# Kernel tuning notes

Hardware: AMD Instinct MI355X
Metric: run time of the kernel (lower is better)

Reference implementation:

```python
import jax, jax.numpy as jnp
import numpy as np

# SMPL-X kinematic tree (55 joints): parent index per joint, root = -1
PARENTS = np.array([-1, 0, 0, 0, 1, 2, 3, 4, 5, 6, 7, 8, 9, 9, 9, 12, 13, 14,
                    16, 17, 18, 19, 15, 22, 23, 20, 25, 26, 20, 28, 29, 20, 31,
                    32, 20, 34, 35, 20, 37, 38, 21, 40, 41, 21, 43, 44, 21, 46,
                    47, 21, 49, 50, 21, 52, 53], dtype=np.int32)
N_JOINTS = 55
B, T = 32, 2048


def setup_inputs() -> dict:
    key = jax.random.key(0)
    k1, k2 = jax.random.split(key)
    motion = jax.random.normal(k1, (B, T, N_JOINTS, 3, 3), dtype=jnp.float32)
    J = jax.random.normal(k2, (N_JOINTS, 3), dtype=jnp.float32) * 0.2  # rest-pose joints
    return {"motion": motion, "J": J}


def reference(motion, J):
    """Process_3D_Motion.calculate_pos with ignore_joints=[].

    motion: [B, T, N, 3, 3] per-joint rotation matrices
    J:      [N, 3] rest-pose joint locations
    returns posed joint positions [B, T, N, 3] (batch_rigid_transform).
    """
    b, t, n = motion.shape[:3]
    bt = b * t
    rot = motion.reshape(bt, n, 3, 3)

    # relative joint offsets w.r.t. parent (root stays absolute)
    rel = jnp.concatenate([J[:1], J[1:] - J[PARENTS[1:]]], axis=0)  # [N, 3]

    # build homogeneous 4x4 transforms [BT, N, 4, 4]
    trans = jnp.broadcast_to(rel[None, :, :, None], (bt, n, 3, 1))
    top = jnp.concatenate([rot, trans], axis=-1)                    # [BT, N, 3, 4]
    bottom_row = jnp.array([0.0, 0.0, 0.0, 1.0], dtype=motion.dtype)
    bottom = jnp.broadcast_to(bottom_row[None, None, None, :], (bt, n, 1, 4))
    mats = jnp.concatenate([top, bottom], axis=-2)                  # [BT, N, 4, 4]

    # sequential kinematic-chain composition (fixed, small loop over joints)
    chain = [mats[:, 0]]
    for i in range(1, n):
        chain.append(chain[int(PARENTS[i])] @ mats[:, i])
    transforms = jnp.stack(chain, axis=1)                           # [BT, N, 4, 4]

    posed = transforms[:, :, :3, 3]                                 # [BT, N, 3]
    return posed.reshape(b, t, n, 3)
```

## Files before the change

kernel.cpp:

```cpp
#include <hip/hip_runtime.h>

#define NJ 55

__device__ constexpr int kPar[NJ] = {
    -1, 0, 0, 0, 1, 2, 3, 4, 5, 6, 7, 8, 9, 9, 9, 12, 13, 14, 16, 17,
    18, 19, 15, 22, 23, 20, 25, 26, 20, 28, 29, 20, 31, 32, 20, 34, 35,
    20, 37, 38, 21, 40, 41, 21, 43, 44, 21, 46, 47, 21, 49, 50, 21, 52, 53
};

__global__ __launch_bounds__(256)
void fk_kernel(const float* __restrict__ motion,
               const float* __restrict__ Jrest,
               float* __restrict__ out,
               int BT)
{
    __shared__ float rel[NJ * 3];

    if (threadIdx.x < NJ) {
        const int j = threadIdx.x;
        const int p = kPar[j];
        float x = Jrest[j * 3 + 0];
        float y = Jrest[j * 3 + 1];
        float z = Jrest[j * 3 + 2];
        if (p >= 0) {
            x -= Jrest[p * 3 + 0];
            y -= Jrest[p * 3 + 1];
            z -= Jrest[p * 3 + 2];
        }
        rel[j * 3 + 0] = x;
        rel[j * 3 + 1] = y;
        rel[j * 3 + 2] = z;
    }
    __syncthreads();

    const int g = blockIdx.x * blockDim.x + threadIdx.x;
    if (g >= BT) return;

    const float* __restrict__ m = motion + (size_t)g * (NJ * 9);
    float* __restrict__ o = out + (size_t)g * (NJ * 3);

    float R[NJ][9];
    float t[NJ][3];

#pragma unroll
    for (int j = 0; j < NJ; ++j) {
        const float b0 = m[j * 9 + 0];
        const float b1 = m[j * 9 + 1];
        const float b2 = m[j * 9 + 2];
        const float b3 = m[j * 9 + 3];
        const float b4 = m[j * 9 + 4];
        const float b5 = m[j * 9 + 5];
        const float b6 = m[j * 9 + 6];
        const float b7 = m[j * 9 + 7];
        const float b8 = m[j * 9 + 8];

        const float rx = rel[j * 3 + 0];
        const float ry = rel[j * 3 + 1];
        const float rz = rel[j * 3 + 2];

        const int p = kPar[j];
        if (p < 0) {
            R[j][0] = b0; R[j][1] = b1; R[j][2] = b2;
            R[j][3] = b3; R[j][4] = b4; R[j][5] = b5;
            R[j][6] = b6; R[j][7] = b7; R[j][8] = b8;
            t[j][0] = rx;
            t[j][1] = ry;
            t[j][2] = rz;
        } else {
            const float a0 = R[p][0], a1 = R[p][1], a2 = R[p][2];
            const float a3 = R[p][3], a4 = R[p][4], a5 = R[p][5];
            const float a6 = R[p][6], a7 = R[p][7], a8 = R[p][8];

            R[j][0] = a0 * b0 + a1 * b3 + a2 * b6;
            R[j][1] = a0 * b1 + a1 * b4 + a2 * b7;
            R[j][2] = a0 * b2 + a1 * b5 + a2 * b8;
            R[j][3] = a3 * b0 + a4 * b3 + a5 * b6;
            R[j][4] = a3 * b1 + a4 * b4 + a5 * b7;
            R[j][5] = a3 * b2 + a4 * b5 + a5 * b8;
            R[j][6] = a6 * b0 + a7 * b3 + a8 * b6;
            R[j][7] = a6 * b1 + a7 * b4 + a8 * b7;
            R[j][8] = a6 * b2 + a7 * b5 + a8 * b8;

            t[j][0] = a0 * rx + a1 * ry + a2 * rz + t[p][0];
            t[j][1] = a3 * rx + a4 * ry + a5 * rz + t[p][1];
            t[j][2] = a6 * rx + a7 * ry + a8 * rz + t[p][2];
        }

        o[j * 3 + 0] = t[j][0];
        o[j * 3 + 1] = t[j][1];
        o[j * 3 + 2] = t[j][2];
    }
}

extern "C" void kernel_launch(void* const* d_in, const int* in_sizes, int n_in,
                              void* d_out, int out_size, void* d_ws, size_t ws_size,
                              hipStream_t stream) {
    const float* motion = (const float*)d_in[0];
    const float* Jrest  = (const float*)d_in[1];
    float* out = (float*)d_out;

    const int BT = in_sizes[0] / (NJ * 9);

    const int block = 256;
    const int grid = (BT + block - 1) / block;
    fk_kernel<<<grid, block, 0, stream>>>(motion, Jrest, out, BT);
}
```

Before: 262.8 us.

## Stage motion tiles into LDS with async double-buffered loads and coalesced stores

```diff
diff --git a/kernel.cpp b/kernel.cpp
--- a/kernel.cpp
+++ b/kernel.cpp
@@ -1,6 +1,12 @@
 #include <hip/hip_runtime.h>
+#include <stdint.h>
 
-#define NJ 55
+#define NJ   55
+#define JT   5
+#define NT   11
+#define SPB  64
+#define TFL  (JT * 9)
+#define OFL  (JT * 3)
 
 __device__ constexpr int kPar[NJ] = {
     -1, 0, 0, 0, 1, 2, 3, 4, 5, 6, 7, 8, 9, 9, 9, 12, 13, 14, 16, 17,
@@ -8,88 +14,128 @@
     20, 37, 38, 21, 40, 41, 21, 43, 44, 21, 46, 47, 21, 49, 50, 21, 52, 53
 };
 
-__global__ __launch_bounds__(256)
+typedef const __attribute__((address_space(1))) void glb_v;
+typedef __attribute__((address_space(3))) void lds_v;
+
+__global__ __launch_bounds__(64)
 void fk_kernel(const float* __restrict__ motion,
                const float* __restrict__ Jrest,
                float* __restrict__ out,
                int BT)
 {
-    __shared__ float rel[NJ * 3];
+    __shared__ float lds_in[2][SPB * TFL];
+    __shared__ float lds_out[SPB * OFL];
+    __shared__ float lds_rel[NJ * 3];
 
-    if (threadIdx.x < NJ) {
-        const int j = threadIdx.x;
-        const int p = kPar[j];
-        float x = Jrest[j * 3 + 0];
-        float y = Jrest[j * 3 + 1];
-        float z = Jrest[j * 3 + 2];
+    const int lane  = threadIdx.x;
+    const int blk_s = blockIdx.x * SPB;
+
+    if (lane < NJ) {
+        const int p = kPar[lane];
+        float x = Jrest[lane * 3 + 0];
+        float y = Jrest[lane * 3 + 1];
+        float z = Jrest[lane * 3 + 2];
         if (p >= 0) {
             x -= Jrest[p * 3 + 0];
             y -= Jrest[p * 3 + 1];
             z -= Jrest[p * 3 + 2];
         }
-        rel[j * 3 + 0] = x;
-        rel[j * 3 + 1] = y;
-        rel[j * 3 + 2] = z;
+        lds_rel[lane * 3 + 0] = x;
+        lds_rel[lane * 3 + 1] = y;
+        lds_rel[lane * 3 + 2] = z;
     }
     __syncthreads();
 
-    const int g = blockIdx.x * blockDim.x + threadIdx.x;
-    if (g >= BT) return;
+    const float* __restrict__ mbase = motion + (size_t)blk_s * (NJ * 9);
 
-    const float* __restrict__ m = motion + (size_t)g * (NJ * 9);
-    float* __restrict__ o = out + (size_t)g * (NJ * 3);
+#define STAGE(T, BUF)                                                        \
+    do {                                                                     \
+        _Pragma("unroll")                                                    \
+        for (int it = 0; it < TFL; ++it) {                                   \
+            const int idx = it * SPB + lane;                                 \
+            const int s   = idx / TFL;              \
+            const int e   = idx - s * TFL;                                   \
+            const float* gp = mbase + (size_t)s * (NJ * 9) + (T) * TFL + e;  \
+            __builtin_amdgcn_global_load_lds(                                \
+                (glb_v*)gp, (lds_v*)&lds_in[BUF][it * SPB], 4, 0, 0);        \
+        }                                                                    \
+    } while (0)
 
-    float R[NJ][9];
-    float t[NJ][3];
+    float Rw[NJ][9];
+    float tw[NJ][3];
+
+    STAGE(0, 0);
 
 #pragma unroll
-    for (int j = 0; j < NJ; ++j) {
-        const float b0 = m[j * 9 + 0];
-        const float b1 = m[j * 9 + 1];
-        const float b2 = m[j * 9 + 2];
-        const float b3 = m[j * 9 + 3];
-        const float b4 = m[j * 9 + 4];
-        const float b5 = m[j * 9 + 5];
-        const float b6 = m[j * 9 + 6];
-        const float b7 = m[j * 9 + 7];
-        const float b8 = m[j * 9 + 8];
+    for (int t = 0; t < NT; ++t) {
+        if (t < NT - 1) {
+            STAGE(t + 1, (t + 1) & 1);
+            asm volatile("s_waitcnt vmcnt(45)" ::: "memory");
+        } else {
+            asm volatile("s_waitcnt vmcnt(0)" ::: "memory");
+        }
+        __builtin_amdgcn_sched_barrier(0);
 
-        const float rx = rel[j * 3 + 0];
-        const float ry = rel[j * 3 + 1];
-        const float rz = rel[j * 3 + 2];
+        const float* __restrict__ Lin = &lds_in[t & 1][0];
 
-        const int p = kPar[j];
-        if (p < 0) {
-            R[j][0] = b0; R[j][1] = b1; R[j][2] = b2;
-            R[j][3] = b3; R[j][4] = b4; R[j][5] = b5;
-            R[j][6] = b6; R[j][7] = b7; R[j][8] = b8;
-            t[j][0] = rx;
-            t[j][1] = ry;
-            t[j][2] = rz;
-        } else {
-            const float a0 = R[p][0], a1 = R[p][1], a2 = R[p][2];
-            const float a3 = R[p][3], a4 = R[p][4], a5 = R[p][5];
-            const float a6 = R[p][6], a7 = R[p][7], a8 = R[p][8];
+#pragma unroll
+        for (int q = 0; q < JT; ++q) {
+            const int j = t * JT + q;
 
-            R[j][0] = a0 * b0 + a1 * b3 + a2 * b6;
-            R[j][1] = a0 * b1 + a1 * b4 + a2 * b7;
-            R[j][2] = a0 * b2 + a1 * b5 + a2 * b8;
-            R[j][3] = a3 * b0 + a4 * b3 + a5 * b6;
-            R[j][4] = a3 * b1 + a4 * b4 + a5 * b7;
-            R[j][5] = a3 * b2 + a4 * b5 + a5 * b8;
-            R[j][6] = a6 * b0 + a7 * b3 + a8 * b6;
-            R[j][7] = a6 * b1 + a7 * b4 + a8 * b7;
-            R[j][8] = a6 * b2 + a7 * b5 + a8 * b8;
+            const float b0 = Lin[lane * TFL + q * 9 + 0];
+            const float b1 = Lin[lane * TFL + q * 9 + 1];
+            const float b2 = Lin[lane * TFL + q * 9 + 2];
+            const float b3 = Lin[lane * TFL + q * 9 + 3];
+            const float b4 = Lin[lane * TFL + q * 9 + 4];
+            const float b5 = Lin[lane * TFL + q * 9 + 5];
+            const float b6 = Lin[lane * TFL + q * 9 + 6];
+            const float b7 = Lin[lane * TFL + q * 9 + 7];
+            const float b8 = Lin[lane * TFL + q * 9 + 8];
 
-            t[j][0] = a0 * rx + a1 * ry + a2 * rz + t[p][0];
-            t[j][1] = a3 * rx + a4 * ry + a5 * rz + t[p][1];
-            t[j][2] = a6 * rx + a7 * ry + a8 * rz + t[p][2];
+            const float rx = lds_rel[j * 3 + 0];
+            const float ry = lds_rel[j * 3 + 1];
+            const float rz = lds_rel[j * 3 + 2];
+
+            const int p = kPar[j];
+            if (p < 0) {
+                Rw[j][0] = b0; Rw[j][1] = b1; Rw[j][2] = b2;
+                Rw[j][3] = b3; Rw[j][4] = b4; Rw[j][5] = b5;
+                Rw[j][6] = b6; Rw[j][7] = b7; Rw[j][8] = b8;
+                tw[j][0] = rx; tw[j][1] = ry; tw[j][2] = rz;
+            } else {
+                const float a0 = Rw[p][0], a1 = Rw[p][1], a2 = Rw[p][2];
+                const float a3 = Rw[p][3], a4 = Rw[p][4], a5 = Rw[p][5];
+                const float a6 = Rw[p][6], a7 = Rw[p][7], a8 = Rw[p][8];
+
+                Rw[j][0] = a0 * b0 + a1 * b3 + a2 * b6;
+                Rw[j][1] = a0 * b1 + a1 * b4 + a2 * b7;
+                Rw[j][2] = a0 * b2 + a1 * b5 + a2 * b8;
+                Rw[j][3] = a3 * b0 + a4 * b3 + a5 * b6;
+                Rw[j][4] = a3 * b1 + a4 * b4 + a5 * b7;
+                Rw[j][5] = a3 * b2 + a4 * b5 + a5 * b8;
+                Rw[j][6] = a6 * b0 + a7 * b3 + a8 * b6;
+                Rw[j][7] = a6 * b1 + a7 * b4 + a8 * b7;
+                Rw[j][8] = a6 * b2 + a7 * b5 + a8 * b8;
+
+                tw[j][0] = a0 * rx + a1 * ry + a2 * rz + tw[p][0];
+                tw[j][1] = a3 * rx + a4 * ry + a5 * rz + tw[p][1];
+                tw[j][2] = a6 * rx + a7 * ry + a8 * rz + tw[p][2];
+            }
+
+            lds_out[lane * OFL + q * 3 + 0] = tw[j][0];
+            lds_out[lane * OFL + q * 3 + 1] = tw[j][1];
+            lds_out[lane * OFL + q * 3 + 2] = tw[j][2];
         }
 
-        o[j * 3 + 0] = t[j][0];
-        o[j * 3 + 1] = t[j][1];
-        o[j * 3 + 2] = t[j][2];
+#pragma unroll
+        for (int it = 0; it < OFL; ++it) {
+            const int idx = it * SPB + lane;
+            const int s   = idx / OFL;
+            const int e   = idx - s * OFL;
+            out[(size_t)(blk_s + s) * (NJ * 3) + t * OFL + e] = lds_out[idx];
+        }
     }
+#undef STAGE
 }
 
 extern "C" void kernel_launch(void* const* d_in, const int* in_sizes, int n_in,
@@ -101,7 +147,6 @@
 
     const int BT = in_sizes[0] / (NJ * 9);
 
-    const int block = 256;
-    const int grid = (BT + block - 1) / block;
-    fk_kernel<<<grid, block, 0, stream>>>(motion, Jrest, out, BT);
+    const int grid = (BT + SPB - 1) / SPB;
+    fk_kernel<<<grid, SPB, 0, stream>>>(motion, Jrest, out, BT);
 }
```

New measurement: 235.4 us. -10.4%, faster.
